# Kernel tuning notes

Hardware: AMD Instinct MI355X
Metric: run time of the kernel (lower is better)

Reference implementation:

```python
import jax, jax.numpy as jnp
import numpy as np
from jax import lax

B, T = 64, 512
VOCAB, E = 16000, 128
USCRIPT, UE = 64, 16
F, MAX_NGRAM = 128, 5
C = 13  # num_classes


def setup_inputs() -> dict:
    key = jax.random.key(0)
    ks = jax.random.split(key, 18)
    inp = {
        "input_char": jax.random.randint(ks[0], (B, T), 0, VOCAB),
        "input_script": jax.random.randint(ks[1], (B, T), 0, USCRIPT),
        "input_mask": jnp.ones((B, T), dtype=bool),
        "char_emb": jax.random.normal(ks[2], (VOCAB, E), jnp.float32) * 0.02,
        "uscript_emb": jax.random.normal(ks[3], (USCRIPT, UE), jnp.float32) * 0.02,
        "dense_w": jax.random.normal(ks[4], (MAX_NGRAM * F + UE, C), jnp.float32) * 0.05,
        "dense_b": jnp.zeros((C,), jnp.float32),
        "trans": jax.random.normal(ks[5], (C, C), jnp.float32) * 0.1,
        "left_b": jax.random.normal(ks[6], (C,), jnp.float32) * 0.1,
        "right_b": jax.random.normal(ks[7], (C,), jnp.float32) * 0.1,
    }
    for i in range(1, MAX_NGRAM + 1):
        inp[f"conv_w{i}"] = jax.random.normal(ks[7 + i], (i, E, F), jnp.float32) * (1.0 / np.sqrt(i * E))
        inp[f"conv_b{i}"] = jnp.zeros((F,), jnp.float32)
    return inp


def _conv1d_same_relu(x, w, b):
    # x: [B,T,Cin], w: [K,Cin,Cout]
    y = lax.conv_general_dilated(x, w, window_strides=(1,), padding="SAME",
                                 dimension_numbers=("NWC", "WIO", "NWC"))
    return jax.nn.relu(y + b)


def _potentials(input_char, input_script, input_mask, char_emb, uscript_emb,
                conv_ws, conv_bs, dense_w, dense_b, left_b, right_b):
    emb = char_emb[input_char]              # [B,T,E]
    uemb = uscript_emb[input_script]        # [B,T,UE]
    feats = [_conv1d_same_relu(emb, w, b) for w, b in zip(conv_ws, conv_bs)]
    ctx = jnp.concatenate(feats + [uemb], axis=-1)          # [B,T,5F+UE]
    pot = jnp.einsum("btf,fc->btc", ctx, dense_w) + dense_b  # [B,T,C]
    # boundary energies (tfa CRF use_boundary=True): add left_b at first
    # valid step, right_b at last valid step per the mask
    m = input_mask.astype(pot.dtype)[..., None]              # [B,T,1]
    prev_m = jnp.pad(m[:, :-1], ((0, 0), (1, 0), (0, 0)))
    next_m = jnp.pad(m[:, 1:], ((0, 0), (0, 1), (0, 0)))
    pot = pot + m * (1.0 - prev_m) * left_b + m * (1.0 - next_m) * right_b
    return pot


def _viterbi_decode(pot, trans):
    # pot: [B,T,C], trans: [C,C]; full-length sequences (mask all ones)
    def fwd(state, pot_t):
        scores = state[:, :, None] + trans[None]   # [B, prev, cur]
        bp = jnp.argmax(scores, axis=1)            # [B,C]
        state = jnp.max(scores, axis=1) + pot_t    # [B,C]
        return state, bp

    final, bps = lax.scan(fwd, pot[:, 0], jnp.swapaxes(pot[:, 1:], 0, 1))
    last = jnp.argmax(final, axis=-1)              # [B]

    def back(tag, bp_t):
        prev = jnp.take_along_axis(bp_t, tag[:, None], axis=1)[:, 0]
        return prev, prev

    _, tags = lax.scan(back, last, bps, reverse=True)  # [T-1, B], forward order
    decoded = jnp.concatenate([jnp.swapaxes(tags, 0, 1), last[:, None]], axis=1)
    return decoded.astype(jnp.int32)


def reference(input_char, input_script, input_mask, char_emb, uscript_emb,
              conv_w1, conv_b1, conv_w2, conv_b2, conv_w3, conv_b3,
              conv_w4, conv_b4, conv_w5, conv_b5,
              dense_w, dense_b, trans, left_b, right_b):
    conv_ws = [conv_w1, conv_w2, conv_w3, conv_w4, conv_w5]
    conv_bs = [conv_b1, conv_b2, conv_b3, conv_b4, conv_b5]
    pot = _potentials(input_char, input_script, input_mask, char_emb, uscript_emb,
                      conv_ws, conv_bs, dense_w, dense_b, left_b, right_b)
    seq_len = jnp.sum(input_mask.astype(jnp.int32), axis=1)
    decoded = _viterbi_decode(pot, trans)
    return decoded, pot, seq_len, trans
```

## Files before the change

kernel.cpp:

```cpp
#include <hip/hip_runtime.h>

#define NB 64
#define NT 512
#define NC 13
#define AP 136
#define WP 72
#define USTRIDE 18432
#define DWT_H   552960
#define DWT_L   563200
#define WS_NEED 1146880

typedef short s8v __attribute__((ext_vector_type(8)));
typedef float f4v __attribute__((ext_vector_type(4)));
typedef unsigned short ush;
typedef unsigned int u32;

__device__ __forceinline__ ush f2bf(float f){
    union { float f; u32 u; } v; v.f = f;
    u32 r = v.u + 0x7fffu + ((v.u >> 16) & 1u);
    return (ush)(r >> 16);
}
__device__ __forceinline__ float bf2f(ush h){
    union { u32 u; float f; } v; v.u = ((u32)h) << 16; return v.f;
}

__global__ __launch_bounds__(512)
void prep_kernel(const float* __restrict__ cw1, const float* __restrict__ cw2,
                 const float* __restrict__ cw3, const float* __restrict__ cw4,
                 const float* __restrict__ cw5, const float* __restrict__ dense_w,
                 ush* __restrict__ ws)
{
    int bx = blockIdx.x, tid = threadIdx.x;
    if (bx < 30) {
        int u = bx, ut = u >> 1, eh = u & 1;
        int fb = ut<1?0: ut<3?1: ut<6?2: ut<10?3:4;
        int jj = ut - fb*(fb+1)/2;
        const float* cw = fb==0?cw1: fb==1?cw2: fb==2?cw3: fb==3?cw4: cw5;
        #pragma unroll
        for (int it = 0; it < 2; ++it) {
            int g = it*512 + tid;
            int f = g & 127;
            int e8 = (g >> 7) << 3;
            float v[8];
            #pragma unroll
            for (int q = 0; q < 8; ++q)
                v[q] = cw[(jj*128 + eh*64 + e8 + q)*128 + f];
            ush h8[8], l8[8];
            #pragma unroll
            for (int q = 0; q < 8; ++q) {
                h8[q] = f2bf(v[q]);
                l8[q] = f2bf(v[q] - bf2f(h8[q]));
            }
            uint4 hv, lv;
            hv.x = h8[0] | ((u32)h8[1]<<16); hv.y = h8[2] | ((u32)h8[3]<<16);
            hv.z = h8[4] | ((u32)h8[5]<<16); hv.w = h8[6] | ((u32)h8[7]<<16);
            lv.x = l8[0] | ((u32)l8[1]<<16); lv.y = l8[2] | ((u32)l8[3]<<16);
            lv.z = l8[4] | ((u32)l8[5]<<16); lv.w = l8[6] | ((u32)l8[7]<<16);
            *(uint4*)&ws[u*USTRIDE + f*WP + e8]        = hv;
            *(uint4*)&ws[u*USTRIDE + 9216 + f*WP + e8] = lv;
        }
    } else {
        int fb = bx - 30;
        #pragma unroll
        for (int it = 0; it < 4; ++it) {
            int idx = it*512 + tid;
            int c = idx >> 7, f = idx & 127;
            float v = (c < 13) ? dense_w[(fb*128 + f)*13 + c] : 0.f;
            ush hi = f2bf(v);
            ws[DWT_H + fb*2048 + idx] = hi;
            ws[DWT_L + fb*2048 + idx] = f2bf(v - bf2f(hi));
        }
    }
}

__global__ __launch_bounds__(512)
void pot_kernel_ws(const int* __restrict__ input_char,
                   const int* __restrict__ input_script,
                   const float* __restrict__ char_emb,
                   const float* __restrict__ uscript_emb,
                   const float* __restrict__ dense_w,
                   const float* __restrict__ dense_b,
                   const float* __restrict__ left_b,
                   const float* __restrict__ right_b,
                   const float* __restrict__ cb1, const float* __restrict__ cb2,
                   const float* __restrict__ cb3, const float* __restrict__ cb4,
                   const float* __restrict__ cb5,
                   const ush* __restrict__ ws,
                   float* __restrict__ out_pot)
{
    __shared__ __align__(16) ush smem[77280];
    ush* Ah     = smem;
    ush* Al     = smem + 17952;
    ush* feat_h = smem + 54336;
    ush* feat_l = smem + 63040;
    float* uebt = (float*)(smem + 72768);
    float* dwue = (float*)(smem + 76864);

    const int tid  = threadIdx.x;
    const int lane = tid & 63;
    const int wid  = tid >> 6;
    const int tg   = wid >> 2;
    const int fg   = wid & 3;
    const int lr   = lane & 15;
    const int lq   = lane >> 4;
    const int bb   = blockIdx.x >> 2;
    const int t0   = (blockIdx.x & 3) << 7;

    {
        const char* g = (const char*)ws;
        char* l = (char*)(smem + 35904);
        #pragma unroll
        for (int i = 0; i < 5; ++i) {
            int idx = wid + (i << 3);
            if (i < 4 || wid < 4)
                __builtin_amdgcn_global_load_lds(
                    (const __attribute__((address_space(1))) void*)(g + idx*1024 + lane*16),
                    (__attribute__((address_space(3))) void*)(l + idx*1024 + lane*16), 16, 0, 0);
        }
    }

    for (int i = tid; i < 132*16; i += 512) {
        int row = i >> 4, s = (i & 15) << 3;
        int t = t0 + row - 2;
        uint4 hv = {0,0,0,0}, lv = {0,0,0,0};
        if (t >= 0 && t < NT) {
            int ch = input_char[bb*NT + t];
            const float* src = char_emb + ch*128 + s;
            float4 x0 = *(const float4*)src;
            float4 x1 = *(const float4*)(src + 4);
            float fs[8] = {x0.x,x0.y,x0.z,x0.w,x1.x,x1.y,x1.z,x1.w};
            ush h[8], l[8];
            #pragma unroll
            for (int q = 0; q < 8; ++q) {
                h[q] = f2bf(fs[q]);
                l[q] = f2bf(fs[q] - bf2f(h[q]));
            }
            hv.x = h[0] | ((u32)h[1]<<16); hv.y = h[2] | ((u32)h[3]<<16);
            hv.z = h[4] | ((u32)h[5]<<16); hv.w = h[6] | ((u32)h[7]<<16);
            lv.x = l[0] | ((u32)l[1]<<16); lv.y = l[2] | ((u32)l[3]<<16);
            lv.z = l[4] | ((u32)l[5]<<16); lv.w = l[6] | ((u32)l[7]<<16);
        }
        *(uint4*)&Ah[row*AP + s] = hv;
        *(uint4*)&Al[row*AP + s] = lv;
    }
    for (int i = tid; i < 2048; i += 512) {
        int uu = i >> 7, tl = i & 127;
        uebt[uu*128 + tl] = uscript_emb[input_script[bb*NT + t0 + tl]*16 + uu];
    }
    if (tid < 208) dwue[tid] = dense_w[640*13 + tid];
    __syncthreads();

    const float* cbs[5] = {cb1, cb2, cb3, cb4, cb5};

    f4v cacc[4][2];
    #pragma unroll
    for (int mt = 0; mt < 4; ++mt)
        #pragma unroll
        for (int nt = 0; nt < 2; ++nt) cacc[mt][nt] = (f4v){0.f,0.f,0.f,0.f};
    f4v dacc = (f4v){0.f,0.f,0.f,0.f};

    #pragma unroll 1
    for (int u = 0; u < 30; ++u) {
        int ut  = u >> 1, eh = u & 1;
        int fb  = ut<1?0: ut<3?1: ut<6?2: ut<10?3:4;
        int jj  = ut - fb*(fb+1)/2;
        int jsh = (2 - (fb >> 1)) + jj;

        if (u < 29) {
            const char* g = (const char*)ws + (u + 1)*36864;
            char* l = (char*)(smem + (((u + 1) & 1) ? 54336 : 35904));
            #pragma unroll
            for (int i = 0; i < 5; ++i) {
                int idx = wid + (i << 3);
                if (i < 4 || wid < 4)
                    __builtin_amdgcn_global_load_lds(
                        (const __attribute__((address_space(1))) void*)(g + idx*1024 + lane*16),
                        (__attribute__((address_space(3))) void*)(l + idx*1024 + lane*16), 16, 0, 0);
            }
        }

        const ush* Wh = smem + ((u & 1) ? 54336 : 35904);
        const ush* Wl = Wh + 9216;
        #pragma unroll
        for (int kk = 0; kk < 2; ++kk) {
            int ko = kk*32 + (lq << 3);
            s8v bh[2], bl[2];
            #pragma unroll
            for (int nt = 0; nt < 2; ++nt) {
                int frow = fg*32 + nt*16 + lr;
                bh[nt] = *(const s8v*)&Wh[frow*WP + ko];
                bl[nt] = *(const s8v*)&Wl[frow*WP + ko];
            }
            #pragma unroll
            for (int mt = 0; mt < 4; ++mt) {
                int row = tg*64 + mt*16 + lr + jsh;
                int ai  = row*AP + eh*64 + ko;
                s8v ah = *(const s8v*)&Ah[ai];
                s8v al = *(const s8v*)&Al[ai];
                #pragma unroll
                for (int nt = 0; nt < 2; ++nt) {
                    cacc[mt][nt] = __builtin_amdgcn_mfma_f32_16x16x32_bf16(ah, bh[nt], cacc[mt][nt], 0,0,0);
                    cacc[mt][nt] = __builtin_amdgcn_mfma_f32_16x16x32_bf16(ah, bl[nt], cacc[mt][nt], 0,0,0);
                    cacc[mt][nt] = __builtin_amdgcn_mfma_f32_16x16x32_bf16(al, bh[nt], cacc[mt][nt], 0,0,0);
                }
            }
        }

        if (u == 1 || u == 5 || u == 11 || u == 19 || u == 29) {
            __syncthreads();
            float cbv0 = cbs[fb][fg*32 + lr];
            float cbv1 = cbs[fb][fg*32 + 16 + lr];

            #pragma unroll 1
            for (int h = 0; h < 2; ++h) {
                if (tg == h) {
                    #pragma unroll
                    for (int mt = 0; mt < 4; ++mt)
                        #pragma unroll
                        for (int nt = 0; nt < 2; ++nt)
                            #pragma unroll
                            for (int r = 0; r < 4; ++r) {
                                float v = fmaxf(cacc[mt][nt][r] + (nt ? cbv1 : cbv0), 0.f);
                                int rw = mt*16 + (lq << 2) + r;
                                int f  = fg*32 + nt*16 + lr;
                                ush hh = f2bf(v);
                                feat_h[rw*AP + f] = hh;
                                feat_l[rw*AP + f] = f2bf(v - bf2f(hh));
                            }
                }
                __syncthreads();
                if (tg == h) {
                    int trow = fg*16 + lr;
                    #pragma unroll
                    for (int kf = 0; kf < 4; ++kf) {
                        int f0 = kf*32 + (lq << 3);
                        s8v a2h = *(const s8v*)&ws[DWT_H + fb*2048 + lr*128 + f0];
                        s8v a2l = *(const s8v*)&ws[DWT_L + fb*2048 + lr*128 + f0];
                        s8v b2h = *(const s8v*)&feat_h[trow*AP + f0];
                        s8v b2l = *(const s8v*)&feat_l[trow*AP + f0];
                        dacc = __builtin_amdgcn_mfma_f32_16x16x32_bf16(a2h, b2h, dacc, 0,0,0);
                        dacc = __builtin_amdgcn_mfma_f32_16x16x32_bf16(a2h, b2l, dacc, 0,0,0);
                        dacc = __builtin_amdgcn_mfma_f32_16x16x32_bf16(a2l, b2h, dacc, 0,0,0);
                    }
                    if (fb == 4) {
                        int tloc  = tg*64 + fg*16 + lr;
                        int tglob = t0 + tloc;
                        float pc[4];
                        #pragma unroll
                        for (int r = 0; r < 4; ++r) pc[r] = dacc[r];
                        #pragma unroll
                        for (int uu = 0; uu < 16; ++uu) {
                            float uv = uebt[uu*128 + tloc];
                            #pragma unroll
                            for (int r = 0; r < 4; ++r) {
                                int c = (lq << 2) + r;
                                if (c < 13) pc[r] = fmaf(uv, dwue[uu*13 + c], pc[r]);
                            }
                        }
                        #pragma unroll
                        for (int r = 0; r < 4; ++r) {
                            int c = (lq << 2) + r;
                            if (c < 13) {
                                float v = pc[r] + dense_b[c];
                                if (tglob == 0)    v += left_b[c];
                                if (tglob == NT-1) v += right_b[c];
                                out_pot[(bb*NT + tglob)*13 + c] = v;
                            }
                        }
                    }
                }
                __syncthreads();
            }
            #pragma unroll
            for (int mt = 0; mt < 4; ++mt)
                #pragma unroll
                for (int nt = 0; nt < 2; ++nt) cacc[mt][nt] = (f4v){0.f,0.f,0.f,0.f};
        } else {
            __syncthreads();
        }
    }
}

__global__ __launch_bounds__(512)
void pot_kernel_fb(const int* __restrict__ input_char,
                   const int* __restrict__ input_script,
                   const float* __restrict__ char_emb,
                   const float* __restrict__ uscript_emb,
                   const float* __restrict__ dense_w,
                   const float* __restrict__ dense_b,
                   const float* __restrict__ left_b,
                   const float* __restrict__ right_b,
                   const float* __restrict__ cw1, const float* __restrict__ cb1,
                   const float* __restrict__ cw2, const float* __restrict__ cb2,
                   const float* __restrict__ cw3, const float* __restrict__ cb3,
                   const float* __restrict__ cw4, const float* __restrict__ cb4,
                   const float* __restrict__ cw5, const float* __restrict__ cb5,
                   float* __restrict__ out_pot)
{
    __shared__ __align__(16) ush smem[71744];
    ush* Ah     = smem;
    ush* Al     = smem + 17952;
    ush* Wh     = smem + 35904;
    ush* Wl     = smem + 45120;
    ush* feat_h = smem + 54336;
    ush* feat_l = smem + 63040;
    float* dwlds = (float*)(smem + 35904);
    float* dwue  = (float*)(smem + 39232);
    float* uebt  = (float*)(smem + 39648);

    const int tid  = threadIdx.x;
    const int lane = tid & 63;
    const int wid  = tid >> 6;
    const int tg   = wid >> 2;
    const int fg   = wid & 3;
    const int lr   = lane & 15;
    const int lq   = lane >> 4;
    const int bb   = blockIdx.x >> 2;
    const int t0   = (blockIdx.x & 3) << 7;

    for (int i = tid; i < 132*16; i += 512) {
        int row = i >> 4, s = (i & 15) << 3;
        int t = t0 + row - 2;
        uint4 hv = {0,0,0,0}, lv = {0,0,0,0};
        if (t >= 0 && t < NT) {
            int ch = input_char[bb*NT + t];
            const float* src = char_emb + ch*128 + s;
            float4 x0 = *(const float4*)src;
            float4 x1 = *(const float4*)(src + 4);
            float fs[8] = {x0.x,x0.y,x0.z,x0.w,x1.x,x1.y,x1.z,x1.w};
            ush h[8], l[8];
            #pragma unroll
            for (int q = 0; q < 8; ++q) {
                h[q] = f2bf(fs[q]);
                l[q] = f2bf(fs[q] - bf2f(h[q]));
            }
            hv.x = h[0] | ((u32)h[1]<<16); hv.y = h[2] | ((u32)h[3]<<16);
            hv.z = h[4] | ((u32)h[5]<<16); hv.w = h[6] | ((u32)h[7]<<16);
            lv.x = l[0] | ((u32)l[1]<<16); lv.y = l[2] | ((u32)l[3]<<16);
            lv.z = l[4] | ((u32)l[5]<<16); lv.w = l[6] | ((u32)l[7]<<16);
        }
        *(uint4*)&Ah[row*AP + s] = hv;
        *(uint4*)&Al[row*AP + s] = lv;
    }

    const float* cws[5] = {cw1, cw2, cw3, cw4, cw5};
    const float* cbs[5] = {cb1, cb2, cb3, cb4, cb5};

    f4v cacc[4][2];
    #pragma unroll
    for (int mt = 0; mt < 4; ++mt)
        #pragma unroll
        for (int nt = 0; nt < 2; ++nt) cacc[mt][nt] = (f4v){0.f,0.f,0.f,0.f};
    f4v dacc = (f4v){0.f,0.f,0.f,0.f};

    #pragma unroll 1
    for (int u = 0; u < 30; ++u) {
        int ut  = u >> 1, eh = u & 1;
        int fb  = ut<1?0: ut<3?1: ut<6?2: ut<10?3:4;
        int jj  = ut - fb*(fb+1)/2;
        int jsh = (2 - (fb >> 1)) + jj;
        const float* cw = cws[fb] + (jj*128 + eh*64)*128;

        __syncthreads();
        for (int g = tid; g < 1024; g += 512) {
            int f = g & 127, e8 = (g >> 7) << 3;
            float v[8];
            #pragma unroll
            for (int q = 0; q < 8; ++q) v[q] = cw[(e8 + q)*128 + f];
            ush h8[8], l8[8];
            #pragma unroll
            for (int q = 0; q < 8; ++q) {
                h8[q] = f2bf(v[q]);
                l8[q] = f2bf(v[q] - bf2f(h8[q]));
            }
            uint4 hv, lv;
            hv.x = h8[0] | ((u32)h8[1]<<16); hv.y = h8[2] | ((u32)h8[3]<<16);
            hv.z = h8[4] | ((u32)h8[5]<<16); hv.w = h8[6] | ((u32)h8[7]<<16);
            lv.x = l8[0] | ((u32)l8[1]<<16); lv.y = l8[2] | ((u32)l8[3]<<16);
            lv.z = l8[4] | ((u32)l8[5]<<16); lv.w = l8[6] | ((u32)l8[7]<<16);
            *(uint4*)&Wh[f*WP + e8] = hv;
            *(uint4*)&Wl[f*WP + e8] = lv;
        }
        __syncthreads();

        #pragma unroll
        for (int kk = 0; kk < 2; ++kk) {
            int ko = kk*32 + (lq << 3);
            s8v bh[2], bl[2];
            #pragma unroll
            for (int nt = 0; nt < 2; ++nt) {
                int frow = fg*32 + nt*16 + lr;
                bh[nt] = *(const s8v*)&Wh[frow*WP + ko];
                bl[nt] = *(const s8v*)&Wl[frow*WP + ko];
            }
            #pragma unroll
            for (int mt = 0; mt < 4; ++mt) {
                int row = tg*64 + mt*16 + lr + jsh;
                int ai  = row*AP + eh*64 + ko;
                s8v ah = *(const s8v*)&Ah[ai];
                s8v al = *(const s8v*)&Al[ai];
                #pragma unroll
                for (int nt = 0; nt < 2; ++nt) {
                    cacc[mt][nt] = __builtin_amdgcn_mfma_f32_16x16x32_bf16(ah, bh[nt], cacc[mt][nt], 0,0,0);
                    cacc[mt][nt] = __builtin_amdgcn_mfma_f32_16x16x32_bf16(ah, bl[nt], cacc[mt][nt], 0,0,0);
                    cacc[mt][nt] = __builtin_amdgcn_mfma_f32_16x16x32_bf16(al, bh[nt], cacc[mt][nt], 0,0,0);
                }
            }
        }

        if (u == 1 || u == 5 || u == 11 || u == 19 || u == 29) {
            __syncthreads();
            for (int i = tid; i < 128*13; i += 512)
                dwlds[i] = dense_w[fb*128*13 + i];
            if (fb == 4) {
                for (int i = tid; i < 16*13; i += 512)
                    dwue[i] = dense_w[640*13 + i];
                for (int i = tid; i < 2048; i += 512) {
                    int uu = i >> 7, tl = i & 127;
                    uebt[uu*128 + tl] = uscript_emb[input_script[bb*NT + t0 + tl]*16 + uu];
                }
            }
            __syncthreads();

            float cbv0 = cbs[fb][fg*32 + lr];
            float cbv1 = cbs[fb][fg*32 + 16 + lr];

            #pragma unroll 1
            for (int h = 0; h < 2; ++h) {
                if (tg == h) {
                    #pragma unroll
                    for (int mt = 0; mt < 4; ++mt)
                        #pragma unroll
                        for (int nt = 0; nt < 2; ++nt)
                            #pragma unroll
                            for (int r = 0; r < 4; ++r) {
                                float v = fmaxf(cacc[mt][nt][r] + (nt ? cbv1 : cbv0), 0.f);
                                int rw = mt*16 + (lq << 2) + r;
                                int f  = fg*32 + nt*16 + lr;
                                ush hh = f2bf(v);
                                feat_h[rw*AP + f] = hh;
                                feat_l[rw*AP + f] = f2bf(v - bf2f(hh));
                            }
                }
                __syncthreads();
                if (tg == h) {
                    int trow = fg*16 + lr;
                    #pragma unroll
                    for (int kf = 0; kf < 4; ++kf) {
                        int f0 = kf*32 + (lq << 3);
                        float dv[8];
                        #pragma unroll
                        for (int q = 0; q < 8; ++q) dv[q] = dwlds[(f0 + q)*13 + lr];
                        s8v a2h, a2l;
                        #pragma unroll
                        for (int q = 0; q < 8; ++q) {
                            ush hh = f2bf(dv[q]);
                            a2h[q] = (short)hh;
                            a2l[q] = (short)f2bf(dv[q] - bf2f(hh));
                        }
                        s8v b2h = *(const s8v*)&feat_h[trow*AP + f0];
                        s8v b2l = *(const s8v*)&feat_l[trow*AP + f0];
                        dacc = __builtin_amdgcn_mfma_f32_16x16x32_bf16(a2h, b2h, dacc, 0,0,0);
                        dacc = __builtin_amdgcn_mfma_f32_16x16x32_bf16(a2h, b2l, dacc, 0,0,0);
                        dacc = __builtin_amdgcn_mfma_f32_16x16x32_bf16(a2l, b2h, dacc, 0,0,0);
                    }
                    if (fb == 4) {
                        int tloc  = tg*64 + fg*16 + lr;
                        int tglob = t0 + tloc;
                        float pc[4];
                        #pragma unroll
                        for (int r = 0; r < 4; ++r) pc[r] = dacc[r];
                        #pragma unroll
                        for (int uu = 0; uu < 16; ++uu) {
                            float uv = uebt[uu*128 + tloc];
                            #pragma unroll
                            for (int r = 0; r < 4; ++r) {
                                int c = (lq << 2) + r;
                                if (c < 13) pc[r] = fmaf(uv, dwue[uu*13 + c], pc[r]);
                            }
                        }
                        #pragma unroll
                        for (int r = 0; r < 4; ++r) {
                            int c = (lq << 2) + r;
                            if (c < 13) {
                                float v = pc[r] + dense_b[c];
                                if (tglob == 0)    v += left_b[c];
                                if (tglob == NT-1) v += right_b[c];
                                out_pot[(bb*NT + tglob)*13 + c] = v;
                            }
                        }
                    }
                }
                __syncthreads();
            }
            #pragma unroll
            for (int mt = 0; mt < 4; ++mt)
                #pragma unroll
                for (int nt = 0; nt < 2; ++nt) cacc[mt][nt] = (f4v){0.f,0.f,0.f,0.f};
        }
    }
}

__global__ __launch_bounds__(256)
void viterbi_kernel(const float* __restrict__ pot,
                    const float* __restrict__ trans,
                    float* __restrict__ out_dec,
                    float* __restrict__ out_seq,
                    float* __restrict__ out_trans)
{
    __shared__ __align__(16) float s_lds[NT * NC];
    __shared__ float t_lds[NC * NC];
    __shared__ unsigned char path_lds[16 * 13 * 32];
    __shared__ unsigned char entry_lds[16 * 13];
    __shared__ int chunk_e[16];

    const int b   = blockIdx.x;
    const int tid = threadIdx.x;

    {
        const float4* src = reinterpret_cast<const float4*>(pot + b * NT * NC);
        float4* dst = reinterpret_cast<float4*>(s_lds);
        for (int i = tid; i < NT * NC / 4; i += 256) dst[i] = src[i];
        for (int i = tid; i < NC * NC; i += 256) t_lds[i] = trans[i];
    }
    __syncthreads();

    if (tid < 64) {
        const int c = tid;
        const bool act = c < NC;
        float tc[13];
        #pragma unroll
        for (int p = 0; p < NC; ++p) tc[p] = t_lds[p * NC + (act ? c : 0)];
        float s = act ? s_lds[c] : -1e30f;

        for (int t = 1; t < NT; ++t) {
            float v[13];
            #pragma unroll
            for (int p = 0; p < NC; ++p) v[p] = __shfl(s, p) + tc[p];
            float m0 = fmaxf(fmaxf(v[0], v[1]), fmaxf(v[2], v[3]));
            float m1 = fmaxf(fmaxf(v[4], v[5]), fmaxf(v[6], v[7]));
            float m2 = fmaxf(fmaxf(v[8], v[9]), fmaxf(v[10], v[11]));
            float best = fmaxf(fmaxf(m0, m1), fmaxf(m2, v[12]));
            float pv = act ? s_lds[t * NC + c] : 0.f;
            s = best + pv;
            if (act) s_lds[t * NC + c] = s;
        }
    }
    __syncthreads();

    if (tid < 16 * 13) {
        const int chunk = tid / 13;
        const int e     = tid - chunk * 13;
        unsigned char* path = &path_lds[(chunk * 13 + e) * 32];
        int cur = e;
        path[31] = (unsigned char)e;
        for (int tl = 31; tl >= 1; --tl) {
            const float* srow = &s_lds[(chunk * 32 + tl - 1) * NC];
            float best = -1e30f; int bi = 0;
            #pragma unroll
            for (int p = 0; p < NC; ++p) {
                float v = srow[p] + t_lds[p * NC + cur];
                if (v > best) { best = v; bi = p; }
            }
            cur = bi;
            path[tl - 1] = (unsigned char)cur;
        }
        if (chunk > 0) {
            const float* srow = &s_lds[(chunk * 32 - 1) * NC];
            float best = -1e30f; int bi = 0;
            #pragma unroll
            for (int p = 0; p < NC; ++p) {
                float v = srow[p] + t_lds[p * NC + cur];
                if (v > best) { best = v; bi = p; }
            }
            entry_lds[chunk * 13 + e] = (unsigned char)bi;
        }
    }
    __syncthreads();

    if (tid == 0) {
        float best = -1e30f; int last = 0;
        for (int c = 0; c < NC; ++c) {
            float v = s_lds[(NT - 1) * NC + c];
            if (v > best) { best = v; last = c; }
        }
        chunk_e[15] = last;
        for (int i = 15; i >= 1; --i)
            chunk_e[i - 1] = entry_lds[i * 13 + chunk_e[i]];
    }
    __syncthreads();

    float* dec = out_dec + b * NT;
    for (int t = tid; t < NT; t += 256) {
        int ck = t >> 5;
        dec[t] = (float)path_lds[(ck * 13 + chunk_e[ck]) * 32 + (t & 31)];
    }
    if (tid == 0) out_seq[b] = (float)NT;
    if (b == 0) {
        for (int i = tid; i < NC * NC; i += 256) out_trans[i] = trans[i];
    }
}

extern "C" void kernel_launch(void* const* d_in, const int* in_sizes, int n_in,
                              void* d_out, int out_size, void* d_ws, size_t ws_size,
                              hipStream_t stream) {
    const int*   input_char   = (const int*)d_in[0];
    const int*   input_script = (const int*)d_in[1];
    const float* char_emb     = (const float*)d_in[3];
    const float* uscript_emb  = (const float*)d_in[4];
    const float* dense_w      = (const float*)d_in[5];
    const float* dense_b      = (const float*)d_in[6];
    const float* trans        = (const float*)d_in[7];
    const float* left_b       = (const float*)d_in[8];
    const float* right_b      = (const float*)d_in[9];
    const float* cw1 = (const float*)d_in[10];
    const float* cb1 = (const float*)d_in[11];
    const float* cw2 = (const float*)d_in[12];
    const float* cb2 = (const float*)d_in[13];
    const float* cw3 = (const float*)d_in[14];
    const float* cb3 = (const float*)d_in[15];
    const float* cw4 = (const float*)d_in[16];
    const float* cb4 = (const float*)d_in[17];
    const float* cw5 = (const float*)d_in[18];
    const float* cb5 = (const float*)d_in[19];

    float* out       = (float*)d_out;
    float* out_dec   = out;
    float* out_pot   = out + NB * NT;
    float* out_seq   = out_pot + NB * NT * NC;
    float* out_trans = out_seq + NB;

    if (ws_size >= (size_t)WS_NEED) {
        hipLaunchKernelGGL(prep_kernel, dim3(35), dim3(512), 0, stream,
                           cw1, cw2, cw3, cw4, cw5, dense_w, (ush*)d_ws);
        hipLaunchKernelGGL(pot_kernel_ws, dim3(256), dim3(512), 0, stream,
                           input_char, input_script, char_emb, uscript_emb,
                           dense_w, dense_b, left_b, right_b,
                           cb1, cb2, cb3, cb4, cb5,
                           (const ush*)d_ws, out_pot);
    } else {
        hipLaunchKernelGGL(pot_kernel_fb, dim3(256), dim3(512), 0, stream,
                           input_char, input_script, char_emb, uscript_emb,
                           dense_w, dense_b, left_b, right_b,
                           cw1, cb1, cw2, cb2, cw3, cb3, cw4, cb4, cw5, cb5,
                           out_pot);
    }

    hipLaunchKernelGGL(viterbi_kernel, dim3(NB), dim3(256), 0, stream,
                       out_pot, trans, out_dec, out_seq, out_trans);
}
```

Measured before the change: 163.4 us.

## Use DPP row rotation for Viterbi max-plus recurrence with transposed potentials

```diff
diff --git a/kernel.cpp b/kernel.cpp
--- a/kernel.cpp
+++ b/kernel.cpp
@@ -5,6 +5,7 @@
 #define NC 13
 #define AP 136
 #define WP 72
+#define PT 516
 #define USTRIDE 18432
 #define DWT_H   552960
 #define DWT_L   563200
@@ -509,6 +510,7 @@
                     float* __restrict__ out_trans)
 {
     __shared__ __align__(16) float s_lds[NT * NC];
+    __shared__ __align__(16) float ptld[16 * PT];
     __shared__ float t_lds[NC * NC];
     __shared__ unsigned char path_lds[16 * 13 * 32];
     __shared__ unsigned char entry_lds[16 * 13];
@@ -517,33 +519,53 @@
     const int b   = blockIdx.x;
     const int tid = threadIdx.x;
 
-    {
-        const float4* src = reinterpret_cast<const float4*>(pot + b * NT * NC);
-        float4* dst = reinterpret_cast<float4*>(s_lds);
-        for (int i = tid; i < NT * NC / 4; i += 256) dst[i] = src[i];
-        for (int i = tid; i < NC * NC; i += 256) t_lds[i] = trans[i];
-    }
+    for (int i = tid; i < 3 * PT; i += 256) ptld[13 * PT + i] = 0.f;
+    for (int i = tid; i < NT * NC; i += 256) {
+        int t = i / NC, c = i - t * NC;
+        float v = pot[b * NT * NC + i];
+        ptld[c * PT + t] = v;
+        if (t == 0) s_lds[c] = v;
+    }
+    for (int i = tid; i < NC * NC; i += 256) t_lds[i] = trans[i];
     __syncthreads();
 
-    if (tid < 64) {
+    if (tid < 16) {
         const int c = tid;
-        const bool act = c < NC;
-        float tc[13];
-        #pragma unroll
-        for (int p = 0; p < NC; ++p) tc[p] = t_lds[p * NC + (act ? c : 0)];
-        float s = act ? s_lds[c] : -1e30f;
-
-        for (int t = 1; t < NT; ++t) {
-            float v[13];
-            #pragma unroll
-            for (int p = 0; p < NC; ++p) v[p] = __shfl(s, p) + tc[p];
-            float m0 = fmaxf(fmaxf(v[0], v[1]), fmaxf(v[2], v[3]));
-            float m1 = fmaxf(fmaxf(v[4], v[5]), fmaxf(v[6], v[7]));
-            float m2 = fmaxf(fmaxf(v[8], v[9]), fmaxf(v[10], v[11]));
-            float best = fmaxf(fmaxf(m0, m1), fmaxf(m2, v[12]));
-            float pv = act ? s_lds[t * NC + c] : 0.f;
-            s = best + pv;
-            if (act) s_lds[t * NC + c] = s;
+        int r1 = __builtin_amdgcn_mov_dpp(c, 0x121, 0xF, 0xF, false);
+        const bool fwd = (r1 == ((c + 1) & 15));
+        float tc[16];
+        #pragma unroll
+        for (int k = 0; k < 16; ++k) {
+            int p = fwd ? ((c + k) & 15) : ((c - k) & 15);
+            tc[k] = (c < 13 && p < 13) ? t_lds[p * NC + c] : -1e30f;
+        }
+        float s = (c < 13) ? s_lds[c] : -1e30f;
+        int t = 1;
+
+        auto step = [&](float pv) {
+            float acc = s + tc[0];
+            float r = s;
+            #pragma unroll
+            for (int k = 1; k < 16; ++k) {
+                r = __int_as_float(__builtin_amdgcn_mov_dpp(
+                        __float_as_int(r), 0x121, 0xF, 0xF, false));
+                acc = fmaxf(acc, r + tc[k]);
+            }
+            s = acc + pv;
+            if (c < 13) s_lds[t * NC + c] = s;
+            ++t;
+        };
+
+        const float* prow = &ptld[c * PT];
+        float4 pvv = *(const float4*)&prow[4];
+        step(prow[1]);
+        step(prow[2]);
+        step(prow[3]);
+        #pragma unroll 1
+        for (int t4 = 4; t4 < NT; t4 += 4) {
+            float4 cur = pvv;
+            if (t4 + 4 < NT) pvv = *(const float4*)&prow[t4 + 4];
+            step(cur.x); step(cur.y); step(cur.z); step(cur.w);
         }
     }
     __syncthreads();
```

Measured after the change: 157.4 us. -3.7%, faster.
